# Kernel tuning notes

Measured on AMD Instinct MI355X. Metric: run time of the kernel, lower is better.

## Reference

```python
import jax, jax.numpy as jnp
import numpy as np

BATCH, VOCAB = 256, 50257

def setup_inputs() -> dict:
    key = jax.random.key(0)
    k1, k2 = jax.random.split(key)
    logits = jax.random.normal(k1, (BATCH, VOCAB), dtype=jnp.float32) * 4.0  # LM-like logit spread
    temperature = jax.random.uniform(k2, (), dtype=jnp.float32, minval=0.5, maxval=1.5)
    return {"logits": logits, "temperature": temperature, "top_k": 50}


def reference(logits, temperature, top_k):
    # temperature scale (dividing by 1.0 is identical to the torch skip-branch)
    scaled = logits / temperature
    # top-k mask: keep exactly the k selected positions, -inf elsewhere
    top_vals, top_idx = jax.lax.top_k(scaled, top_k)          # [B, k]
    b = jnp.arange(scaled.shape[0])[:, None]                  # [B, 1]
    masked = jnp.full_like(scaled, -jnp.inf).at[b, top_idx].set(top_vals)
    # softmax + multinomial(num_samples=1) == categorical over masked logits
    key = jax.random.key(42)
    sampled = jax.random.categorical(key, masked, axis=-1)    # [B]
    return sampled
```

## Files before the change

### kernel.cpp

```cpp
#include <hip/hip_runtime.h>
#include <stdint.h>


#define VOCAB 50257
#define BATCH 256
#define NT 1024
#define NBINS 4096
#define CAND_CAP 2048
#define FILTER_VAL 4.0f

__device__ __forceinline__ uint32_t rotl32(uint32_t v, int r) {
  return (v << r) | (v >> (32 - r));
}

__device__ __forceinline__ void threefry2x32_42(uint32_t& x0, uint32_t& x1) {
  const uint32_t ks0 = 0u;
  const uint32_t ks1 = 42u;
  const uint32_t ks2 = ks0 ^ ks1 ^ 0x1BD11BDAu;
  x0 += ks0; x1 += ks1;
#define TF_R(r) { x0 += x1; x1 = rotl32(x1, (r)); x1 ^= x0; }
  TF_R(13) TF_R(15) TF_R(26) TF_R(6)
  x0 += ks1; x1 += ks2 + 1u;
  TF_R(17) TF_R(29) TF_R(16) TF_R(24)
  x0 += ks2; x1 += ks0 + 2u;
  TF_R(13) TF_R(15) TF_R(26) TF_R(6)
  x0 += ks0; x1 += ks1 + 3u;
  TF_R(17) TF_R(29) TF_R(16) TF_R(24)
  x0 += ks1; x1 += ks2 + 4u;
  TF_R(13) TF_R(15) TF_R(26) TF_R(6)
  x0 += ks2; x1 += ks0 + 5u;
#undef TF_R
}

__device__ __forceinline__ float gumbel_at(uint32_t flat) {
  uint32_t x0 = 0u, x1 = flat;
  threefry2x32_42(x0, x1);
  uint32_t bits = x0 ^ x1;
  uint32_t fb = (bits >> 9) | 0x3f800000u;
  float f = __uint_as_float(fb) - 1.0f;
  float u = fmaxf(f, 1.17549435e-38f);
  float t = (float)log((double)u);
  float g = (float)(-log((double)(-t)));
  return g;
}

__device__ __forceinline__ uint32_t fkey(float x) {
  uint32_t u = __float_as_uint(x);
  return (u & 0x80000000u) ? ~u : (u | 0x80000000u);
}

extern "C" __global__ void __launch_bounds__(NT)
topk_sample_kernel(const float* __restrict__ logits,
                   const float* __restrict__ temp_p,
                   const int* __restrict__ topk_p,
                   int* __restrict__ out) {
  const int row = blockIdx.x;
  const int tid = threadIdx.x;
  const float temp = temp_p[0];
  const int K = topk_p[0];
  const float* rowp = logits + (size_t)row * VOCAB;

  const int pc = (4 - (row & 3)) & 3;
  const int nv4 = (VOCAB - pc) >> 2;
  const int tailbase = pc + (nv4 << 2);
  const int tailc = VOCAB - tailbase;
  const float4* body = (const float4*)(rowp + pc);

  __shared__ unsigned hist[NBINS];
  __shared__ unsigned wtot[16];
  __shared__ unsigned aboveWave[16];
  __shared__ int sh_tb, sh_total, sh_cnt;
  __shared__ unsigned ckey[CAND_CAP];
  __shared__ int cidx[CAND_CAP];
  __shared__ float red_v[NT];
  __shared__ int red_i[NT];

  const int lane = tid & 63;
  const int wave = tid >> 6;

  uint32_t filt = fkey(FILTER_VAL);
  int tb = 0;
  for (;;) {
    for (int b = tid; b < NBINS; b += NT) hist[b] = 0u;
    __syncthreads();
    if (tid < pc) {
      uint32_t k = fkey(rowp[tid]);
      if (k >= filt) atomicAdd(&hist[k >> 20], 1u);
    }
    for (int v = tid; v < nv4; v += NT) {
      float4 x = body[v];
      uint32_t k0 = fkey(x.x), k1 = fkey(x.y), k2 = fkey(x.z), k3 = fkey(x.w);
      if (k0 >= filt) atomicAdd(&hist[k0 >> 20], 1u);
      if (k1 >= filt) atomicAdd(&hist[k1 >> 20], 1u);
      if (k2 >= filt) atomicAdd(&hist[k2 >> 20], 1u);
      if (k3 >= filt) atomicAdd(&hist[k3 >> 20], 1u);
    }
    if (tid < tailc) {
      uint32_t k = fkey(rowp[tailbase + tid]);
      if (k >= filt) atomicAdd(&hist[k >> 20], 1u);
    }
    __syncthreads();

    unsigned p = hist[4 * tid] + hist[4 * tid + 1] + hist[4 * tid + 2] + hist[4 * tid + 3];
    unsigned v = p;
    for (int off = 1; off < 64; off <<= 1) {
      unsigned o = (unsigned)__shfl_down((int)v, off);
      if (lane + off < 64) v += o;
    }
    if (lane == 0) wtot[wave] = v;
    __syncthreads();
    if (tid == 0) {
      unsigned acc = 0;
      for (int w = 15; w >= 0; --w) { aboveWave[w] = acc; acc += wtot[w]; }
      sh_total = (int)acc;
    }
    __syncthreads();
    unsigned above = aboveWave[wave] + (v - p);
    if (above < (unsigned)K && above + p >= (unsigned)K) {
      int need = K - (int)above;
      for (int b = 3; b >= 0; --b) {
        unsigned c = hist[4 * tid + b];
        if (c >= (unsigned)need) { sh_tb = 4 * tid + b; break; }
        need -= (int)c;
      }
    }
    __syncthreads();
    if (sh_total >= K) { tb = sh_tb; break; }
    filt = 0u;
    __syncthreads();
  }

  const uint32_t cutk = (uint32_t)max(tb - 1, 0) << 20;
  if (tid == 0) sh_cnt = 0;
  __syncthreads();
  if (tid < pc) {
    if (fkey(rowp[tid]) >= cutk) {
      int p = atomicAdd(&sh_cnt, 1);
      if (p < CAND_CAP) cidx[p] = tid;
    }
  }
  for (int v = tid; v < nv4; v += NT) {
    float4 x = body[v];
    int base = pc + (v << 2);
    if (fkey(x.x) >= cutk) { int p = atomicAdd(&sh_cnt, 1); if (p < CAND_CAP) cidx[p] = base; }
    if (fkey(x.y) >= cutk) { int p = atomicAdd(&sh_cnt, 1); if (p < CAND_CAP) cidx[p] = base + 1; }
    if (fkey(x.z) >= cutk) { int p = atomicAdd(&sh_cnt, 1); if (p < CAND_CAP) cidx[p] = base + 2; }
    if (fkey(x.w) >= cutk) { int p = atomicAdd(&sh_cnt, 1); if (p < CAND_CAP) cidx[p] = base + 3; }
  }
  if (tid < tailc) {
    if (fkey(rowp[tailbase + tid]) >= cutk) {
      int p = atomicAdd(&sh_cnt, 1);
      if (p < CAND_CAP) cidx[p] = tailbase + tid;
    }
  }
  __syncthreads();
  const int C = min(sh_cnt, CAND_CAP);

  if (tid < C) {
    int idx = cidx[tid];
    float s = rowp[idx] / temp;
    ckey[tid] = fkey(s);
  }
  __syncthreads();

  float bestv = -__builtin_huge_valf();
  int besti = 0x7fffffff;
  if (tid < C) {
    const uint32_t mk = ckey[tid];
    const int mi = cidx[tid];
    int rank = 0;
    for (int j = 0; j < C; ++j) {
      uint32_t k = ckey[j];
      rank += (k > mk || (k == mk && cidx[j] < mi)) ? 1 : 0;
    }
    if (rank < K) {
      float s = rowp[mi] / temp;
      float v = s + gumbel_at((uint32_t)row * (uint32_t)VOCAB + (uint32_t)mi);
      bestv = v; besti = mi;
    }
  }

  red_v[tid] = bestv;
  red_i[tid] = besti;
  __syncthreads();
  for (int off = NT / 2; off > 0; off >>= 1) {
    if (tid < off) {
      float v2 = red_v[tid + off];
      int i2 = red_i[tid + off];
      if (v2 > red_v[tid] || (v2 == red_v[tid] && i2 < red_i[tid])) {
        red_v[tid] = v2;
        red_i[tid] = i2;
      }
    }
    __syncthreads();
  }
  if (tid == 0) out[row] = red_i[0];
}

extern "C" void kernel_launch(void* const* d_in, const int* in_sizes, int n_in,
                              void* d_out, int out_size, void* d_ws, size_t ws_size,
                              hipStream_t stream) {
  const float* logits = (const float*)d_in[0];
  const float* temp_p = (const float*)d_in[1];
  const int* topk_p = (const int*)d_in[2];
  int* out = (int*)d_out;
  hipLaunchKernelGGL(topk_sample_kernel, dim3(BATCH), dim3(NT), 0, stream,
                     logits, temp_p, topk_p, out);
}
```

Before: 103.5 us.

## Add speculative single-pass top-k using fixed logit threshold with verified fallback

Before doing any histogram work, the kernel collects candidates whose raw logit is at least a fixed threshold (10.0) in one pass, ranks them, and checks that the K-th largest scaled value exceeds the scaled threshold. If the check passes, the histogram threshold-search pass and the second collection pass are skipped. If it fails, the original histogram-based path runs. The final argmax reduction also moves from a 1024-entry shared-memory tree to wave shuffles plus a 16-entry final step. The fast path depends on the input's logit distribution to hit often, and adds an extra pass whenever it misses.

```diff
diff --git a/kernel.cpp b/kernel.cpp
--- a/kernel.cpp
+++ b/kernel.cpp
@@ -8,6 +8,7 @@
 #define NBINS 4096
 #define CAND_CAP 2048
 #define FILTER_VAL 4.0f
+#define SPEC_VAL 10.0f
 
 __device__ __forceinline__ uint32_t rotl32(uint32_t v, int r) {
   return (v << r) | (v >> (32 - r));
@@ -69,72 +70,23 @@
   __shared__ unsigned hist[NBINS];
   __shared__ unsigned wtot[16];
   __shared__ unsigned aboveWave[16];
-  __shared__ int sh_tb, sh_total, sh_cnt;
+  __shared__ int sh_tb, sh_total, sh_cnt, sh_ok;
   __shared__ unsigned ckey[CAND_CAP];
   __shared__ int cidx[CAND_CAP];
-  __shared__ float red_v[NT];
-  __shared__ int red_i[NT];
+  __shared__ float wbv[16];
+  __shared__ int wbi[16];
 
   const int lane = tid & 63;
   const int wave = tid >> 6;
 
-  uint32_t filt = fkey(FILTER_VAL);
-  int tb = 0;
-  for (;;) {
-    for (int b = tid; b < NBINS; b += NT) hist[b] = 0u;
-    __syncthreads();
-    if (tid < pc) {
-      uint32_t k = fkey(rowp[tid]);
-      if (k >= filt) atomicAdd(&hist[k >> 20], 1u);
-    }
-    for (int v = tid; v < nv4; v += NT) {
-      float4 x = body[v];
-      uint32_t k0 = fkey(x.x), k1 = fkey(x.y), k2 = fkey(x.z), k3 = fkey(x.w);
-      if (k0 >= filt) atomicAdd(&hist[k0 >> 20], 1u);
-      if (k1 >= filt) atomicAdd(&hist[k1 >> 20], 1u);
-      if (k2 >= filt) atomicAdd(&hist[k2 >> 20], 1u);
-      if (k3 >= filt) atomicAdd(&hist[k3 >> 20], 1u);
-    }
-    if (tid < tailc) {
-      uint32_t k = fkey(rowp[tailbase + tid]);
-      if (k >= filt) atomicAdd(&hist[k >> 20], 1u);
-    }
-    __syncthreads();
-
-    unsigned p = hist[4 * tid] + hist[4 * tid + 1] + hist[4 * tid + 2] + hist[4 * tid + 3];
-    unsigned v = p;
-    for (int off = 1; off < 64; off <<= 1) {
-      unsigned o = (unsigned)__shfl_down((int)v, off);
-      if (lane + off < 64) v += o;
-    }
-    if (lane == 0) wtot[wave] = v;
-    __syncthreads();
-    if (tid == 0) {
-      unsigned acc = 0;
-      for (int w = 15; w >= 0; --w) { aboveWave[w] = acc; acc += wtot[w]; }
-      sh_total = (int)acc;
-    }
-    __syncthreads();
-    unsigned above = aboveWave[wave] + (v - p);
-    if (above < (unsigned)K && above + p >= (unsigned)K) {
-      int need = K - (int)above;
-      for (int b = 3; b >= 0; --b) {
-        unsigned c = hist[4 * tid + b];
-        if (c >= (unsigned)need) { sh_tb = 4 * tid + b; break; }
-        need -= (int)c;
-      }
-    }
-    __syncthreads();
-    if (sh_total >= K) { tb = sh_tb; break; }
-    filt = 0u;
-    __syncthreads();
-  }
-
-  const uint32_t cutk = (uint32_t)max(tb - 1, 0) << 20;
-  if (tid == 0) sh_cnt = 0;
+  float bestv = -__builtin_huge_valf();
+  int besti = 0x7fffffff;
+  bool done = false;
+
+  if (tid == 0) { sh_cnt = 0; sh_ok = 0; }
   __syncthreads();
   if (tid < pc) {
-    if (fkey(rowp[tid]) >= cutk) {
+    if (rowp[tid] >= SPEC_VAL) {
       int p = atomicAdd(&sh_cnt, 1);
       if (p < CAND_CAP) cidx[p] = tid;
     }
@@ -142,59 +94,173 @@
   for (int v = tid; v < nv4; v += NT) {
     float4 x = body[v];
     int base = pc + (v << 2);
-    if (fkey(x.x) >= cutk) { int p = atomicAdd(&sh_cnt, 1); if (p < CAND_CAP) cidx[p] = base; }
-    if (fkey(x.y) >= cutk) { int p = atomicAdd(&sh_cnt, 1); if (p < CAND_CAP) cidx[p] = base + 1; }
-    if (fkey(x.z) >= cutk) { int p = atomicAdd(&sh_cnt, 1); if (p < CAND_CAP) cidx[p] = base + 2; }
-    if (fkey(x.w) >= cutk) { int p = atomicAdd(&sh_cnt, 1); if (p < CAND_CAP) cidx[p] = base + 3; }
+    if (x.x >= SPEC_VAL) { int p = atomicAdd(&sh_cnt, 1); if (p < CAND_CAP) cidx[p] = base; }
+    if (x.y >= SPEC_VAL) { int p = atomicAdd(&sh_cnt, 1); if (p < CAND_CAP) cidx[p] = base + 1; }
+    if (x.z >= SPEC_VAL) { int p = atomicAdd(&sh_cnt, 1); if (p < CAND_CAP) cidx[p] = base + 2; }
+    if (x.w >= SPEC_VAL) { int p = atomicAdd(&sh_cnt, 1); if (p < CAND_CAP) cidx[p] = base + 3; }
   }
   if (tid < tailc) {
-    if (fkey(rowp[tailbase + tid]) >= cutk) {
+    if (rowp[tailbase + tid] >= SPEC_VAL) {
       int p = atomicAdd(&sh_cnt, 1);
       if (p < CAND_CAP) cidx[p] = tailbase + tid;
     }
   }
   __syncthreads();
-  const int C = min(sh_cnt, CAND_CAP);
-
-  if (tid < C) {
-    int idx = cidx[tid];
-    float s = rowp[idx] / temp;
-    ckey[tid] = fkey(s);
-  }
+  const int total = sh_cnt;
+
+  if (total >= K && total <= CAND_CAP) {
+    const int C = total;
+    float s_mine = 0.0f;
+    if (tid < C) {
+      s_mine = rowp[cidx[tid]] / temp;
+      ckey[tid] = fkey(s_mine);
+    }
+    __syncthreads();
+    if (tid < C) {
+      const uint32_t mk = ckey[tid];
+      const int mi = cidx[tid];
+      int rank = 0;
+      for (int j = 0; j < C; ++j) {
+        uint32_t k = ckey[j];
+        rank += (k > mk || (k == mk && cidx[j] < mi)) ? 1 : 0;
+      }
+      if (rank == K - 1) {
+        sh_ok = (mk > fkey(SPEC_VAL / temp)) ? 1 : 0;
+      }
+      if (rank < K) {
+        float v = s_mine + gumbel_at((uint32_t)row * (uint32_t)VOCAB + (uint32_t)mi);
+        bestv = v; besti = mi;
+      }
+    }
+    __syncthreads();
+    if (sh_ok) {
+      done = true;
+    } else {
+      bestv = -__builtin_huge_valf();
+      besti = 0x7fffffff;
+    }
+  }
+
+  if (!done) {
+    uint32_t filt = fkey(FILTER_VAL);
+    int tb = 0;
+    for (;;) {
+      for (int b = tid; b < NBINS; b += NT) hist[b] = 0u;
+      __syncthreads();
+      if (tid < pc) {
+        uint32_t k = fkey(rowp[tid]);
+        if (k >= filt) atomicAdd(&hist[k >> 20], 1u);
+      }
+      for (int v = tid; v < nv4; v += NT) {
+        float4 x = body[v];
+        uint32_t k0 = fkey(x.x), k1 = fkey(x.y), k2 = fkey(x.z), k3 = fkey(x.w);
+        if (k0 >= filt) atomicAdd(&hist[k0 >> 20], 1u);
+        if (k1 >= filt) atomicAdd(&hist[k1 >> 20], 1u);
+        if (k2 >= filt) atomicAdd(&hist[k2 >> 20], 1u);
+        if (k3 >= filt) atomicAdd(&hist[k3 >> 20], 1u);
+      }
+      if (tid < tailc) {
+        uint32_t k = fkey(rowp[tailbase + tid]);
+        if (k >= filt) atomicAdd(&hist[k >> 20], 1u);
+      }
+      __syncthreads();
+
+      unsigned p = hist[4 * tid] + hist[4 * tid + 1] + hist[4 * tid + 2] + hist[4 * tid + 3];
+      unsigned v = p;
+      for (int off = 1; off < 64; off <<= 1) {
+        unsigned o = (unsigned)__shfl_down((int)v, off);
+        if (lane + off < 64) v += o;
+      }
+      if (lane == 0) wtot[wave] = v;
+      __syncthreads();
+      if (tid == 0) {
+        unsigned acc = 0;
+        for (int w = 15; w >= 0; --w) { aboveWave[w] = acc; acc += wtot[w]; }
+        sh_total = (int)acc;
+      }
+      __syncthreads();
+      unsigned above = aboveWave[wave] + (v - p);
+      if (above < (unsigned)K && above + p >= (unsigned)K) {
+        int need = K - (int)above;
+        for (int b = 3; b >= 0; --b) {
+          unsigned c = hist[4 * tid + b];
+          if (c >= (unsigned)need) { sh_tb = 4 * tid + b; break; }
+          need -= (int)c;
+        }
+      }
+      __syncthreads();
+      if (sh_total >= K) { tb = sh_tb; break; }
+      filt = 0u;
+      __syncthreads();
+    }
+
+    const uint32_t cutk = (uint32_t)max(tb - 1, 0) << 20;
+    if (tid == 0) sh_cnt = 0;
+    __syncthreads();
+    if (tid < pc) {
+      if (fkey(rowp[tid]) >= cutk) {
+        int p = atomicAdd(&sh_cnt, 1);
+        if (p < CAND_CAP) cidx[p] = tid;
+      }
+    }
+    for (int v = tid; v < nv4; v += NT) {
+      float4 x = body[v];
+      int base = pc + (v << 2);
+      if (fkey(x.x) >= cutk) { int p = atomicAdd(&sh_cnt, 1); if (p < CAND_CAP) cidx[p] = base; }
+      if (fkey(x.y) >= cutk) { int p = atomicAdd(&sh_cnt, 1); if (p < CAND_CAP) cidx[p] = base + 1; }
+      if (fkey(x.z) >= cutk) { int p = atomicAdd(&sh_cnt, 1); if (p < CAND_CAP) cidx[p] = base + 2; }
+      if (fkey(x.w) >= cutk) { int p = atomicAdd(&sh_cnt, 1); if (p < CAND_CAP) cidx[p] = base + 3; }
+    }
+    if (tid < tailc) {
+      if (fkey(rowp[tailbase + tid]) >= cutk) {
+        int p = atomicAdd(&sh_cnt, 1);
+        if (p < CAND_CAP) cidx[p] = tailbase + tid;
+      }
+    }
+    __syncthreads();
+    const int C = min(sh_cnt, CAND_CAP);
+
+    if (tid < C) {
+      int idx = cidx[tid];
+      float s = rowp[idx] / temp;
+      ckey[tid] = fkey(s);
+    }
+    __syncthreads();
+
+    if (tid < C) {
+      const uint32_t mk = ckey[tid];
+      const int mi = cidx[tid];
+      int rank = 0;
+      for (int j = 0; j < C; ++j) {
+        uint32_t k = ckey[j];
+        rank += (k > mk || (k == mk && cidx[j] < mi)) ? 1 : 0;
+      }
+      if (rank < K) {
+        float s = rowp[mi] / temp;
+        float v = s + gumbel_at((uint32_t)row * (uint32_t)VOCAB + (uint32_t)mi);
+        bestv = v; besti = mi;
+      }
+    }
+    __syncthreads();
+  }
+
+  for (int off = 32; off > 0; off >>= 1) {
+    float v2 = __shfl_down(bestv, off);
+    int i2 = __shfl_down(besti, off);
+    if (v2 > bestv || (v2 == bestv && i2 < besti)) { bestv = v2; besti = i2; }
+  }
+  if (lane == 0) { wbv[wave] = bestv; wbi[wave] = besti; }
   __syncthreads();
-
-  float bestv = -__builtin_huge_valf();
-  int besti = 0x7fffffff;
-  if (tid < C) {
-    const uint32_t mk = ckey[tid];
-    const int mi = cidx[tid];
-    int rank = 0;
-    for (int j = 0; j < C; ++j) {
-      uint32_t k = ckey[j];
-      rank += (k > mk || (k == mk && cidx[j] < mi)) ? 1 : 0;
-    }
-    if (rank < K) {
-      float s = rowp[mi] / temp;
-      float v = s + gumbel_at((uint32_t)row * (uint32_t)VOCAB + (uint32_t)mi);
-      bestv = v; besti = mi;
-    }
-  }
-
-  red_v[tid] = bestv;
-  red_i[tid] = besti;
-  __syncthreads();
-  for (int off = NT / 2; off > 0; off >>= 1) {
-    if (tid < off) {
-      float v2 = red_v[tid + off];
-      int i2 = red_i[tid + off];
-      if (v2 > red_v[tid] || (v2 == red_v[tid] && i2 < red_i[tid])) {
-        red_v[tid] = v2;
-        red_i[tid] = i2;
-      }
-    }
-    __syncthreads();
-  }
-  if (tid == 0) out[row] = red_i[0];
+  if (tid == 0) {
+    float bv = wbv[0];
+    int bi = wbi[0];
+    for (int w = 1; w < 16; ++w) {
+      float v2 = wbv[w];
+      int i2 = wbi[w];
+      if (v2 > bv || (v2 == bv && i2 < bi)) { bv = v2; bi = i2; }
+    }
+    out[row] = bi;
+  }
 }
 
 extern "C" void kernel_launch(void* const* d_in, const int* in_sizes, int n_in,
```

Result: slower. 118.7 us (+14.7%).
